# Optimization experiments

Measured on AMD Instinct MI355X. Metric: run time of the kernel, lower is better.

The kernel has to match this reference:

```python
import jax, jax.numpy as jnp
import numpy as np

NEG = -1e30  # finite stand-in for -inf so logaddexp grads stay clean
ADVERSARY_WEIGHT = 0.5


def _bfctc(logits, targets, act_lens, tgt_lens):
    """Blank-free CTC negative log-likelihood, size_average=True (mean over batch).

    logits: (T, B, C) unnormalized activations (log_softmax applied internally,
            as in warp-ctc style bindings).
    targets: (B, U) int label ids (padding beyond tgt_lens is ignored).
    Alignment lattice: at each frame stay on the same label or advance one
    label (no blank state):
        alpha[t, u] = logaddexp(alpha[t-1, u], alpha[t-1, u-1]) + logp[t, y_u]
    Loss per utterance = -alpha[act_len-1, tgt_len-1].
    """
    T, B, C = logits.shape
    U = targets.shape[1]
    logprobs = jax.nn.log_softmax(logits, axis=-1)  # (T,B,C)
    idx = jnp.broadcast_to(targets[None], (T, B, U))
    lp = jnp.take_along_axis(logprobs, idx, axis=2)  # (T,B,U) logp of each target label per frame

    alpha0 = lp[0] + jnp.where(jnp.arange(U) == 0, 0.0, NEG)[None, :]  # (B,U)

    def step(alpha, inp):
        lp_t, t = inp
        shifted = jnp.concatenate(
            [jnp.full((B, 1), NEG, alpha.dtype), alpha[:, :-1]], axis=1)
        new = jnp.logaddexp(alpha, shifted) + lp_t
        # freeze alpha once past this utterance's frame length
        alpha = jnp.where((t < act_lens)[:, None], new, alpha)
        return alpha, None

    alpha, _ = jax.lax.scan(step, alpha0, (lp[1:], jnp.arange(1, T)))
    loss_b = -jnp.take_along_axis(alpha, (tgt_lens - 1)[:, None], axis=1)[:, 0]
    return jnp.mean(loss_b)  # size_average=True


def reference(x, W, b, ctc_target_p1, ctc_target_p2, ctc_acts_lens,
              ctc_target_lens_p1, ctc_target_lens_p2):
    # output_layer projection then (B,T,C) -> (T,B,C), float32 cast
    logits = (x @ W + b)
    acts = jnp.transpose(logits, (1, 0, 2)).astype(jnp.float32)
    l1 = _bfctc(acts, ctc_target_p1, ctc_acts_lens, ctc_target_lens_p1)
    l2 = _bfctc(acts, ctc_target_p2, ctc_acts_lens, ctc_target_lens_p2)
    return (l1 - ADVERSARY_WEIGHT * l2, l1, l2)


def setup_inputs() -> dict:
    B, T, U, D, C = 16, 2000, 400, 512, 4096
    key = jax.random.key(0)
    k = jax.random.split(key, 8)
    x = jax.random.normal(k[0], (B, T, D), dtype=jnp.float32)
    W = jax.random.normal(k[1], (D, C), dtype=jnp.float32) * 0.02
    b = jnp.zeros((C,), dtype=jnp.float32)
    tgt1 = jax.random.randint(k[2], (B, U), 0, C)
    tgt2 = jax.random.randint(k[3], (B, U), 0, C)
    # frame lengths in [T//2, T) so every target (U<=400) has a valid alignment
    act_lens = jax.random.randint(k[4], (B,), T // 2, T)
    tlen1 = jax.random.randint(k[5], (B,), 1, U + 1)
    tlen2 = jax.random.randint(k[6], (B,), 1, U + 1)
    return {
        "x": x, "W": W, "b": b,
        "ctc_target_p1": tgt1, "ctc_target_p2": tgt2,
        "ctc_acts_lens": act_lens,
        "ctc_target_lens_p1": tlen1, "ctc_target_lens_p2": tlen2,
    }
```

## Files before the change

kernel.cpp:

```cpp
#include <hip/hip_runtime.h>
#include <hip/hip_bf16.h>
#include <stdint.h>

constexpr int B_ = 16;
constexpr int T_ = 2000;
constexpr int U_ = 400;
constexpr int D_ = 512;
constexpr int C_ = 4096;
constexpr int U2P_ = 1024;
constexpr float LN2F = 0.6931471805599453f;

typedef __attribute__((ext_vector_type(8))) short bf16x8;
typedef __attribute__((ext_vector_type(4))) float f32x4;
typedef __attribute__((ext_vector_type(8))) unsigned short us8;

__device__ __forceinline__ ushort f2bf(float f) {
  uint32_t u = __builtin_bit_cast(uint32_t, f);
  uint32_t r = (u + 0x7fffu + ((u >> 16) & 1u)) >> 16;
  return (ushort)r;
}

__device__ __forceinline__ float bf2f(ushort h) {
  return __builtin_bit_cast(float, (uint32_t)h << 16);
}

__device__ __forceinline__ void async_copy16(const void* gptr, void* ldsptr) {
  __builtin_amdgcn_global_load_lds(
      (const __attribute__((address_space(1))) uint32_t*)gptr,
      (__attribute__((address_space(3))) uint32_t*)ldsptr,
      16, 0, 0);
}

__global__ void cvt_bf16_k(const float* __restrict__ in, ushort* __restrict__ out, int n4) {
  int i = blockIdx.x * blockDim.x + threadIdx.x;
  int stride = gridDim.x * blockDim.x;
  for (; i < n4; i += stride) {
    float4 v = ((const float4*)in)[i];
    ushort4 o;
    o.x = f2bf(v.x); o.y = f2bf(v.y); o.z = f2bf(v.z); o.w = f2bf(v.w);
    ((ushort4*)out)[i] = o;
  }
}

__global__ void transposeW_k(const float* __restrict__ W, ushort* __restrict__ Wt) {
  __shared__ float tile[32][33];
  int c0 = blockIdx.x * 32, d0 = blockIdx.y * 32;
  int tx = threadIdx.x, ty = threadIdx.y;
  #pragma unroll
  for (int i = 0; i < 4; ++i) {
    int r = ty + i * 8;
    tile[r][tx] = W[(size_t)(d0 + r) * C_ + c0 + tx];
  }
  __syncthreads();
  #pragma unroll
  for (int i = 0; i < 4; ++i) {
    int r = ty + i * 8;
    Wt[(size_t)(c0 + r) * D_ + d0 + tx] = f2bf(tile[tx][r]);
  }
}

__global__ void gatherW_k(const ushort* __restrict__ Wt, const float* __restrict__ bias,
                          const int* __restrict__ t1, const int* __restrict__ t2,
                          ushort* __restrict__ Wgt, float* __restrict__ biasg) {
  int u2 = blockIdx.x;
  int b = blockIdx.y;
  int tid = threadIdx.x;
  int set = u2 >= 512;
  int us = u2 - (set ? 512 : 0);
  int c = (us < U_) ? (set ? t2 : t1)[b * U_ + us] : -1;
  ushort4 v; v.x = 0; v.y = 0; v.z = 0; v.w = 0;
  if (c >= 0) v = *(const ushort4*)(Wt + (size_t)c * D_ + tid * 4);
  *(ushort4*)(Wgt + ((size_t)b * U2P_ + u2) * D_ + tid * 4) = v;
  if (tid == 0) biasg[b * U2P_ + u2] = (c >= 0) ? bias[c] : 0.f;
}

template <bool IS_LP>
__global__ __launch_bounds__(512, 2) void gemm8_k(
    const ushort* __restrict__ A, const ushort* __restrict__ Bt,
    const float* __restrict__ biasp, float* __restrict__ lsesum,
    ushort* __restrict__ cbuf) {
  constexpr int K = D_;
  __shared__ __align__(16) ushort As[2][2][8192];
  __shared__ __align__(16) ushort Bs[2][2][8192];
  const int tid = threadIdx.x;
  const int wid = tid >> 6, lane = tid & 63;
  const int wr = wid >> 2, wc = wid & 3;
  const int h = lane >> 4, lr = lane & 15;
  const int bn = blockIdx.x, bm = blockIdx.y, bz = blockIdx.z;

  const ushort* Ab = A + ((size_t)(IS_LP ? bz * T_ : 0) + (size_t)bm * 256) * K;
  const ushort* Bb = Bt + ((size_t)(IS_LP ? bz * U2P_ : 0) + (size_t)bn * 256) * K;

  auto frag = [&](const ushort* chunk, int row) -> bf16x8 {
    int c16 = (h + (row >> 1)) & 3;
    return *(const bf16x8*)(chunk + row * 32 + c16 * 8);
  };
  auto stage = [&](ushort* chunk, const ushort* gsrc) {
    #pragma unroll
    for (int j = 0; j < 2; ++j) {
      int o = j * 512 + tid;
      int row = o >> 2;
      int g = ((o & 3) - (row >> 1)) & 3;
      async_copy16(gsrc + (size_t)row * K + g * 8,
                   chunk + (j * 512 + wid * 64) * 8);
    }
  };

  f32x4 acc[8][4];
  #pragma unroll
  for (int mi = 0; mi < 8; ++mi)
    #pragma unroll
    for (int ni = 0; ni < 4; ++ni) {
      f32x4 z = {0.f, 0.f, 0.f, 0.f};
      acc[mi][ni] = z;
    }

  stage(&As[0][0][0], Ab);
  stage(&Bs[0][0][0], Bb);
  stage(&As[0][1][0], Ab + 32);
  stage(&Bs[0][1][0], Bb + 32);

  #pragma unroll 2
  for (int kt = 0; kt < 8; ++kt) {
    const int c = kt & 1, nx = c ^ 1;
    const ushort* A0 = &As[c][0][0];
    const ushort* A1 = &As[c][1][0];
    const ushort* B0 = &Bs[c][0][0];
    const ushort* B1 = &Bs[c][1][0];
    const ushort* Asrc = Ab + (kt + 1) * 64;
    const ushort* Bsrc = Bb + (kt + 1) * 64;
    bf16x8 bf0[4], bf1[4], af[4];

    asm volatile("s_waitcnt vmcnt(4)" ::: "memory");
    __builtin_amdgcn_s_barrier();
    __builtin_amdgcn_sched_barrier(0);
    #pragma unroll
    for (int ni = 0; ni < 4; ++ni) bf0[ni] = frag(B0, wc * 64 + ni * 16 + lr);
    #pragma unroll
    for (int mi = 0; mi < 4; ++mi) af[mi] = frag(A0, wr * 128 + mi * 16 + lr);
    if (kt < 7) stage(&As[nx][0][0], Asrc);
    __builtin_amdgcn_s_setprio(1);
    #pragma unroll
    for (int mi = 0; mi < 4; ++mi)
      #pragma unroll
      for (int ni = 0; ni < 4; ++ni)
        acc[mi][ni] = __builtin_amdgcn_mfma_f32_16x16x32_bf16(af[mi], bf0[ni], acc[mi][ni], 0, 0, 0);
    __builtin_amdgcn_s_setprio(0);

    __builtin_amdgcn_s_barrier();
    __builtin_amdgcn_sched_barrier(0);
    #pragma unroll
    for (int mi = 0; mi < 4; ++mi) af[mi] = frag(A0, wr * 128 + (mi + 4) * 16 + lr);
    if (kt < 7) stage(&Bs[nx][0][0], Bsrc);
    __builtin_amdgcn_s_setprio(1);
    #pragma unroll
    for (int mi = 0; mi < 4; ++mi)
      #pragma unroll
      for (int ni = 0; ni < 4; ++ni)
        acc[mi + 4][ni] = __builtin_amdgcn_mfma_f32_16x16x32_bf16(af[mi], bf0[ni], acc[mi + 4][ni], 0, 0, 0);
    __builtin_amdgcn_s_setprio(0);

    if (kt < 7) { asm volatile("s_waitcnt vmcnt(4)" ::: "memory"); }
    else        { asm volatile("s_waitcnt vmcnt(0)" ::: "memory"); }
    __builtin_amdgcn_s_barrier();
    __builtin_amdgcn_sched_barrier(0);
    #pragma unroll
    for (int ni = 0; ni < 4; ++ni) bf1[ni] = frag(B1, wc * 64 + ni * 16 + lr);
    #pragma unroll
    for (int mi = 0; mi < 4; ++mi) af[mi] = frag(A1, wr * 128 + mi * 16 + lr);
    if (kt < 7) stage(&As[nx][1][0], Asrc + 32);
    __builtin_amdgcn_s_setprio(1);
    #pragma unroll
    for (int mi = 0; mi < 4; ++mi)
      #pragma unroll
      for (int ni = 0; ni < 4; ++ni)
        acc[mi][ni] = __builtin_amdgcn_mfma_f32_16x16x32_bf16(af[mi], bf1[ni], acc[mi][ni], 0, 0, 0);
    __builtin_amdgcn_s_setprio(0);

    __builtin_amdgcn_s_barrier();
    __builtin_amdgcn_sched_barrier(0);
    #pragma unroll
    for (int mi = 0; mi < 4; ++mi) af[mi] = frag(A1, wr * 128 + (mi + 4) * 16 + lr);
    if (kt < 7) stage(&Bs[nx][1][0], Bsrc + 32);
    __builtin_amdgcn_s_setprio(1);
    #pragma unroll
    for (int mi = 0; mi < 4; ++mi)
      #pragma unroll
      for (int ni = 0; ni < 4; ++ni)
        acc[mi + 4][ni] = __builtin_amdgcn_mfma_f32_16x16x32_bf16(af[mi], bf1[ni], acc[mi + 4][ni], 0, 0, 0);
    __builtin_amdgcn_s_setprio(0);
  }

  if constexpr (!IS_LP) {
    float bv[4];
    #pragma unroll
    for (int ni = 0; ni < 4; ++ni)
      bv[ni] = biasp[bn * 256 + wc * 64 + ni * 16 + lr];
    #pragma unroll
    for (int mi = 0; mi < 8; ++mi) {
      #pragma unroll
      for (int r = 0; r < 4; ++r) {
        float s = 0.f;
        #pragma unroll
        for (int ni = 0; ni < 4; ++ni) s += __expf(acc[mi][ni][r] + bv[ni]);
        s += __shfl_xor(s, 1);
        s += __shfl_xor(s, 2);
        s += __shfl_xor(s, 4);
        s += __shfl_xor(s, 8);
        if (lr == 0) {
          int grow = bm * 256 + wr * 128 + mi * 16 + h * 4 + r;
          atomicAdd(&lsesum[grow], s);
        }
      }
    }
  } else {
    float bv[4];
    #pragma unroll
    for (int ni = 0; ni < 4; ++ni)
      bv[ni] = biasp[bz * U2P_ + bn * 256 + wc * 64 + ni * 16 + lr];
    #pragma unroll
    for (int mi = 0; mi < 8; ++mi) {
      #pragma unroll
      for (int r = 0; r < 4; ++r) {
        int t = bm * 256 + wr * 128 + mi * 16 + h * 4 + r;
        if (t < T_) {
          #pragma unroll
          for (int ni = 0; ni < 4; ++ni) {
            int u2 = bn * 256 + wc * 64 + ni * 16 + lr;
            int set = u2 >> 9;
            int us = u2 & 511;
            float val = (us < U_) ? __expf(acc[mi][ni][r] + bv[ni]) : 0.f;
            cbuf[((size_t)(bz * 2 + set) * T_ + t) * 512 + us] = f2bf(val);
          }
        }
      }
    }
  }
}

__global__ void lse_reduce_k(const float* __restrict__ lsesum, const int* __restrict__ act_lens,
                             float* __restrict__ S) {
  int b = blockIdx.x;
  int al = act_lens[b];
  float s = 0.f;
  for (int t = threadIdx.x; t < al; t += blockDim.x)
    s += logf(lsesum[b * T_ + t]);
  #pragma unroll
  for (int off = 32; off >= 1; off >>= 1) s += __shfl_xor(s, off);
  __shared__ float wsum[4];
  int w = threadIdx.x >> 6, lane = threadIdx.x & 63;
  if (lane == 0) wsum[w] = s;
  __syncthreads();
  if (threadIdx.x == 0) S[b] = wsum[0] + wsum[1] + wsum[2] + wsum[3];
}

__global__ __launch_bounds__(64) void bfctc_scan_k(
    const ushort* __restrict__ cbuf, const int* __restrict__ act_lens,
    const int* __restrict__ tl1, const int* __restrict__ tl2,
    float* __restrict__ rawloss) {
  int bi = blockIdx.x;
  int b = bi >> 1, set = bi & 1;
  int lane = threadIdx.x;
  int al = act_lens[b];
  int tl = (set ? tl2 : tl1)[b];
  const char* base = (const char*)cbuf + (size_t)bi * T_ * 1024 + lane * 16;

  float alpha[8];
  int E = 0;
  float bscale;

  {
    us8 c0 = *(const us8*)(base);
    float iv0 = bf2f(c0[0]);
    #pragma unroll
    for (int r = 0; r < 8; ++r) alpha[r] = 0.f;
    if (lane == 0) alpha[0] = iv0;
    bscale = (lane >= 50) ? 0.f : 1.0f;
  }

  auto step1 = [&](us8 c8) {
    int pi = __builtin_amdgcn_update_dpp(
        0, __builtin_bit_cast(int, alpha[7]), 0x138 , 0xf, 0xf, true);
    float prev = __builtin_bit_cast(float, pi) * bscale;
    float c[8];
    #pragma unroll
    for (int r = 0; r < 8; ++r) c[r] = bf2f(c8[r]);
    #pragma unroll
    for (int r = 7; r >= 1; --r)
      alpha[r] = (alpha[r] + alpha[r - 1]) * c[r];
    alpha[0] = (alpha[0] + prev) * c[0];
  };

  auto rescale = [&]() {
    float m01 = fmaxf(alpha[0], alpha[1]);
    float m23 = fmaxf(alpha[2], alpha[3]);
    float m45 = fmaxf(alpha[4], alpha[5]);
    float m67 = fmaxf(alpha[6], alpha[7]);
    float m = fmaxf(fmaxf(m01, m23), fmaxf(m45, m67));
    int mb = __builtin_bit_cast(int, m);
    bool dead = (mb == 0);
    int ei = ((mb >> 23) & 255) - 127;
    float s = __builtin_bit_cast(float, (127 - ei) << 23);
    #pragma unroll
    for (int r = 0; r < 8; ++r) alpha[r] *= s;
    if (!dead) E += ei;
    int pe = __builtin_amdgcn_update_dpp(0, E, 0x138, 0xf, 0xf, true);
    if (dead) E = pe;
    int dE = pe - E;
    dE = dE < -126 ? -126 : (dE > 126 ? 126 : dE);
    bscale = __builtin_bit_cast(float, (127 + dE) << 23);
    if (lane >= 50) bscale = 0.f;
  };

  us8 B0[8], B1[8], B2[8], B3[8];
  auto load0 = [&](int blk) {
    const char* p = base + (size_t)(1 + 8 * blk) * 1024;
    #pragma unroll
    for (int i = 0; i < 8; ++i) B0[i] = *(const us8*)(p + i * 1024);
  };
  auto load1 = [&](int blk) {
    const char* p = base + (size_t)(1 + 8 * blk) * 1024;
    #pragma unroll
    for (int i = 0; i < 8; ++i) B1[i] = *(const us8*)(p + i * 1024);
  };
  auto load2 = [&](int blk) {
    const char* p = base + (size_t)(1 + 8 * blk) * 1024;
    #pragma unroll
    for (int i = 0; i < 8; ++i) B2[i] = *(const us8*)(p + i * 1024);
  };
  auto load3 = [&](int blk) {
    const char* p = base + (size_t)(1 + 8 * blk) * 1024;
    #pragma unroll
    for (int i = 0; i < 8; ++i) B3[i] = *(const us8*)(p + i * 1024);
  };
  auto comp0 = [&]() {
    #pragma unroll
    for (int i = 0; i < 8; ++i) step1(B0[i]);
  };
  auto comp1 = [&]() {
    #pragma unroll
    for (int i = 0; i < 8; ++i) step1(B1[i]);
  };
  auto comp2 = [&]() {
    #pragma unroll
    for (int i = 0; i < 8; ++i) step1(B2[i]);
  };
  auto comp3 = [&]() {
    #pragma unroll
    for (int i = 0; i < 8; ++i) step1(B3[i]);
  };

  int S = al - 1;
  int nb = S >> 3;
  load0(0); load1(1); load2(2); load3(3);
  int j = 0;
  while (j + 4 <= nb) {
    comp0(); rescale(); load0(j + 4);
    comp1(); rescale(); load1(j + 5);
    comp2(); rescale(); load2(j + 6);
    comp3(); rescale(); load3(j + 7);
    j += 4;
  }
  if (j < nb)     { comp0(); rescale(); }
  if (j + 1 < nb) { comp1(); rescale(); }
  if (j + 2 < nb) { comp2(); rescale(); }
  for (int t = 1 + 8 * nb; t <= S; ++t) {
    us8 c = *(const us8*)(base + (size_t)t * 1024);
    step1(c);
  }

  int ui = tl - 1, lt = ui >> 3, rt = ui & 7;
  float v = alpha[0];
  #pragma unroll
  for (int r = 1; r < 8; ++r) v = (rt == r) ? alpha[r] : v;
  float tot = (__builtin_amdgcn_logf(v) + (float)E) * LN2F;
  tot = __shfl(tot, lt);
  if (lane == 0) rawloss[bi] = tot;
}

__global__ void combine_k(const float* __restrict__ S, const float* __restrict__ raw,
                          float* __restrict__ out) {
  int lane = threadIdx.x;
  float d1 = 0.f, d2 = 0.f;
  if (lane < 16) {
    d1 = S[lane] - raw[lane * 2 + 0];
    d2 = S[lane] - raw[lane * 2 + 1];
  }
  #pragma unroll
  for (int off = 8; off >= 1; off >>= 1) {
    d1 += __shfl_xor(d1, off);
    d2 += __shfl_xor(d2, off);
  }
  if (lane == 0) {
    float l1 = d1 * (1.f / 16.f), l2 = d2 * (1.f / 16.f);
    out[0] = l1 - 0.5f * l2;
    out[1] = l1;
    out[2] = l2;
  }
}

extern "C" void kernel_launch(void* const* d_in, const int* in_sizes, int n_in,
                              void* d_out, int out_size, void* d_ws, size_t ws_size,
                              hipStream_t stream) {
  const float* x    = (const float*)d_in[0];
  const float* W    = (const float*)d_in[1];
  const float* bias = (const float*)d_in[2];
  const int* t1  = (const int*)d_in[3];
  const int* t2  = (const int*)d_in[4];
  const int* al  = (const int*)d_in[5];
  const int* tl1 = (const int*)d_in[6];
  const int* tl2 = (const int*)d_in[7];
  float* out = (float*)d_out;

  char* ws = (char*)d_ws;
  size_t off = 0;
  auto alloc = [&](size_t bytes) -> char* {
    char* p = ws + off;
    off += (bytes + 255) & ~(size_t)255;
    return p;
  };
  ushort* xb     = (ushort*)alloc((size_t)B_ * T_ * D_ * 2);
  ushort* Wt     = (ushort*)alloc((size_t)C_ * D_ * 2);
  ushort* Wgt    = (ushort*)alloc((size_t)B_ * U2P_ * D_ * 2);
  float*  biasg  = (float*)alloc((size_t)B_ * U2P_ * 4);
  float*  lsesum = (float*)alloc((size_t)B_ * T_ * 4);
  ushort* cbuf   = (ushort*)alloc((size_t)2 * B_ * T_ * 512 * 2);
  alloc(65536);
  float*  Sb     = (float*)alloc(B_ * 4);
  float*  rawl   = (float*)alloc(2 * B_ * 4);
  (void)ws_size; (void)in_sizes; (void)n_in; (void)out_size;

  (void)hipMemsetAsync(lsesum, 0, (size_t)B_ * T_ * 4, stream);

  cvt_bf16_k<<<2048, 256, 0, stream>>>(x, xb, B_ * T_ * D_ / 4);
  transposeW_k<<<dim3(C_ / 32, D_ / 32), dim3(32, 8), 0, stream>>>(W, Wt);
  gatherW_k<<<dim3(U2P_, B_), 128, 0, stream>>>(Wt, bias, t1, t2, Wgt, biasg);

  gemm8_k<false><<<dim3(C_ / 256, (B_ * T_) / 256, 1), 512, 0, stream>>>(
      xb, Wt, bias, lsesum, nullptr);
  gemm8_k<true><<<dim3(U2P_ / 256, 2048 / 256, B_), 512, 0, stream>>>(
      xb, Wgt, biasg, nullptr, cbuf);

  lse_reduce_k<<<B_, 256, 0, stream>>>(lsesum, al, Sb);
  bfctc_scan_k<<<2 * B_, 64, 0, stream>>>(cbuf, al, tl1, tl2, rawl);
  combine_k<<<1, 64, 0, stream>>>(Sb, rawl, out);
}
```

Measured before the change: 470.4 us.

## Make LSE GEMM blocks loop over eight N tiles with persistent row sums

```diff
diff --git a/kernel.cpp b/kernel.cpp
--- a/kernel.cpp
+++ b/kernel.cpp
@@ -74,11 +74,172 @@
   if (tid == 0) biasg[b * U2P_ + u2] = (c >= 0) ? bias[c] : 0.f;
 }
 
-template <bool IS_LP>
-__global__ __launch_bounds__(512, 2) void gemm8_k(
+__global__ __launch_bounds__(512, 2) void gemm_lse8_k(
     const ushort* __restrict__ A, const ushort* __restrict__ Bt,
-    const float* __restrict__ biasp, float* __restrict__ lsesum,
-    ushort* __restrict__ cbuf) {
+    const float* __restrict__ biasp, float* __restrict__ lsesum) {
+  constexpr int K = D_;
+  __shared__ __align__(16) ushort As[2][2][8192];
+  __shared__ __align__(16) ushort Bs[2][2][8192];
+  const int tid = threadIdx.x;
+  const int wid = tid >> 6, lane = tid & 63;
+  const int wr = wid >> 2, wc = wid & 3;
+  const int h = lane >> 4, lr = lane & 15;
+  const int nh = blockIdx.x;
+  const int bm = blockIdx.y;
+
+  const ushort* Ab = A + (size_t)bm * 256 * K;
+  const ushort* Bbase = Bt + (size_t)nh * 2048 * K;
+
+  auto frag = [&](const ushort* chunk, int row) -> bf16x8 {
+    int c16 = (h + (row >> 1)) & 3;
+    return *(const bf16x8*)(chunk + row * 32 + c16 * 8);
+  };
+  auto stage = [&](ushort* chunk, const ushort* gsrc) {
+    #pragma unroll
+    for (int j = 0; j < 2; ++j) {
+      int o = j * 512 + tid;
+      int row = o >> 2;
+      int g = ((o & 3) - (row >> 1)) & 3;
+      async_copy16(gsrc + (size_t)row * K + g * 8,
+                   chunk + (j * 512 + wid * 64) * 8);
+    }
+  };
+
+  f32x4 acc[8][4];
+  float rowsum[8][4];
+  #pragma unroll
+  for (int mi = 0; mi < 8; ++mi)
+    #pragma unroll
+    for (int ni = 0; ni < 4; ++ni) {
+      f32x4 z = {0.f, 0.f, 0.f, 0.f};
+      acc[mi][ni] = z;
+    }
+  #pragma unroll
+  for (int mi = 0; mi < 8; ++mi)
+    #pragma unroll
+    for (int r = 0; r < 4; ++r) rowsum[mi][r] = 0.f;
+
+  stage(&As[0][0][0], Ab);
+  stage(&Bs[0][0][0], Bbase);
+  stage(&As[0][1][0], Ab + 32);
+  stage(&Bs[0][1][0], Bbase + 32);
+
+  for (int i = 0; i < 64; ++i) {
+    const int c = i & 1, nx = c ^ 1;
+    const int kt1 = (i + 1) & 7, bn1 = (i + 1) >> 3;
+    const ushort* A0 = &As[c][0][0];
+    const ushort* A1 = &As[c][1][0];
+    const ushort* B0 = &Bs[c][0][0];
+    const ushort* B1 = &Bs[c][1][0];
+    const ushort* Asrc = Ab + kt1 * 64;
+    const ushort* Bsrc = Bbase + (size_t)bn1 * 256 * K + kt1 * 64;
+    bf16x8 bf0[4], bf1[4], af[4];
+
+    asm volatile("s_waitcnt vmcnt(4)" ::: "memory");
+    __builtin_amdgcn_s_barrier();
+    __builtin_amdgcn_sched_barrier(0);
+    #pragma unroll
+    for (int ni = 0; ni < 4; ++ni) bf0[ni] = frag(B0, wc * 64 + ni * 16 + lr);
+    #pragma unroll
+    for (int mi = 0; mi < 4; ++mi) af[mi] = frag(A0, wr * 128 + mi * 16 + lr);
+    if (i < 63) stage(&As[nx][0][0], Asrc);
+    __builtin_amdgcn_s_setprio(1);
+    #pragma unroll
+    for (int mi = 0; mi < 4; ++mi)
+      #pragma unroll
+      for (int ni = 0; ni < 4; ++ni)
+        acc[mi][ni] = __builtin_amdgcn_mfma_f32_16x16x32_bf16(af[mi], bf0[ni], acc[mi][ni], 0, 0, 0);
+    __builtin_amdgcn_s_setprio(0);
+
+    __builtin_amdgcn_s_barrier();
+    __builtin_amdgcn_sched_barrier(0);
+    #pragma unroll
+    for (int mi = 0; mi < 4; ++mi) af[mi] = frag(A0, wr * 128 + (mi + 4) * 16 + lr);
+    if (i < 63) stage(&Bs[nx][0][0], Bsrc);
+    __builtin_amdgcn_s_setprio(1);
+    #pragma unroll
+    for (int mi = 0; mi < 4; ++mi)
+      #pragma unroll
+      for (int ni = 0; ni < 4; ++ni)
+        acc[mi + 4][ni] = __builtin_amdgcn_mfma_f32_16x16x32_bf16(af[mi], bf0[ni], acc[mi + 4][ni], 0, 0, 0);
+    __builtin_amdgcn_s_setprio(0);
+
+    if (i < 63) { asm volatile("s_waitcnt vmcnt(4)" ::: "memory"); }
+    else        { asm volatile("s_waitcnt vmcnt(0)" ::: "memory"); }
+    __builtin_amdgcn_s_barrier();
+    __builtin_amdgcn_sched_barrier(0);
+    #pragma unroll
+    for (int ni = 0; ni < 4; ++ni) bf1[ni] = frag(B1, wc * 64 + ni * 16 + lr);
+    #pragma unroll
+    for (int mi = 0; mi < 4; ++mi) af[mi] = frag(A1, wr * 128 + mi * 16 + lr);
+    if (i < 63) stage(&As[nx][1][0], Asrc + 32);
+    __builtin_amdgcn_s_setprio(1);
+    #pragma unroll
+    for (int mi = 0; mi < 4; ++mi)
+      #pragma unroll
+      for (int ni = 0; ni < 4; ++ni)
+        acc[mi][ni] = __builtin_amdgcn_mfma_f32_16x16x32_bf16(af[mi], bf1[ni], acc[mi][ni], 0, 0, 0);
+    __builtin_amdgcn_s_setprio(0);
+
+    __builtin_amdgcn_s_barrier();
+    __builtin_amdgcn_sched_barrier(0);
+    #pragma unroll
+    for (int mi = 0; mi < 4; ++mi) af[mi] = frag(A1, wr * 128 + (mi + 4) * 16 + lr);
+    if (i < 63) stage(&Bs[nx][1][0], Bsrc + 32);
+    __builtin_amdgcn_s_setprio(1);
+    #pragma unroll
+    for (int mi = 0; mi < 4; ++mi)
+      #pragma unroll
+      for (int ni = 0; ni < 4; ++ni)
+        acc[mi + 4][ni] = __builtin_amdgcn_mfma_f32_16x16x32_bf16(af[mi], bf1[ni], acc[mi + 4][ni], 0, 0, 0);
+    __builtin_amdgcn_s_setprio(0);
+
+    if ((i & 7) == 7) {
+      int bn = i >> 3;
+      float bv[4];
+      #pragma unroll
+      for (int ni = 0; ni < 4; ++ni)
+        bv[ni] = biasp[nh * 2048 + bn * 256 + wc * 64 + ni * 16 + lr];
+      #pragma unroll
+      for (int mi = 0; mi < 8; ++mi) {
+        #pragma unroll
+        for (int r = 0; r < 4; ++r) {
+          float s = 0.f;
+          #pragma unroll
+          for (int ni = 0; ni < 4; ++ni) s += __expf(acc[mi][ni][r] + bv[ni]);
+          rowsum[mi][r] += s;
+        }
+      }
+      #pragma unroll
+      for (int mi = 0; mi < 8; ++mi)
+        #pragma unroll
+        for (int ni = 0; ni < 4; ++ni) {
+          f32x4 z = {0.f, 0.f, 0.f, 0.f};
+          acc[mi][ni] = z;
+        }
+    }
+  }
+
+  #pragma unroll
+  for (int mi = 0; mi < 8; ++mi) {
+    #pragma unroll
+    for (int r = 0; r < 4; ++r) {
+      float s = rowsum[mi][r];
+      s += __shfl_xor(s, 1);
+      s += __shfl_xor(s, 2);
+      s += __shfl_xor(s, 4);
+      s += __shfl_xor(s, 8);
+      if (lr == 0) {
+        int grow = bm * 256 + wr * 128 + mi * 16 + h * 4 + r;
+        atomicAdd(&lsesum[grow], s);
+      }
+    }
+  }
+}
+
+__global__ __launch_bounds__(512, 2) void gemm_lp8_k(
+    const ushort* __restrict__ A, const ushort* __restrict__ Bt,
+    const float* __restrict__ biasp, ushort* __restrict__ cbuf) {
   constexpr int K = D_;
   __shared__ __align__(16) ushort As[2][2][8192];
   __shared__ __align__(16) ushort Bs[2][2][8192];
@@ -88,8 +249,8 @@
   const int h = lane >> 4, lr = lane & 15;
   const int bn = blockIdx.x, bm = blockIdx.y, bz = blockIdx.z;
 
-  const ushort* Ab = A + ((size_t)(IS_LP ? bz * T_ : 0) + (size_t)bm * 256) * K;
-  const ushort* Bb = Bt + ((size_t)(IS_LP ? bz * U2P_ : 0) + (size_t)bn * 256) * K;
+  const ushort* Ab = A + ((size_t)bz * T_ + (size_t)bm * 256) * K;
+  const ushort* Bb = Bt + ((size_t)bz * U2P_ + (size_t)bn * 256) * K;
 
   auto frag = [&](const ushort* chunk, int row) -> bf16x8 {
     int c16 = (h + (row >> 1)) & 3;
@@ -191,47 +352,23 @@
     __builtin_amdgcn_s_setprio(0);
   }
 
-  if constexpr (!IS_LP) {
-    float bv[4];
-    #pragma unroll
-    for (int ni = 0; ni < 4; ++ni)
-      bv[ni] = biasp[bn * 256 + wc * 64 + ni * 16 + lr];
-    #pragma unroll
-    for (int mi = 0; mi < 8; ++mi) {
-      #pragma unroll
-      for (int r = 0; r < 4; ++r) {
-        float s = 0.f;
+  float bv[4];
+  #pragma unroll
+  for (int ni = 0; ni < 4; ++ni)
+    bv[ni] = biasp[bz * U2P_ + bn * 256 + wc * 64 + ni * 16 + lr];
+  #pragma unroll
+  for (int mi = 0; mi < 8; ++mi) {
+    #pragma unroll
+    for (int r = 0; r < 4; ++r) {
+      int t = bm * 256 + wr * 128 + mi * 16 + h * 4 + r;
+      if (t < T_) {
         #pragma unroll
-        for (int ni = 0; ni < 4; ++ni) s += __expf(acc[mi][ni][r] + bv[ni]);
-        s += __shfl_xor(s, 1);
-        s += __shfl_xor(s, 2);
-        s += __shfl_xor(s, 4);
-        s += __shfl_xor(s, 8);
-        if (lr == 0) {
-          int grow = bm * 256 + wr * 128 + mi * 16 + h * 4 + r;
-          atomicAdd(&lsesum[grow], s);
-        }
-      }
-    }
-  } else {
-    float bv[4];
-    #pragma unroll
-    for (int ni = 0; ni < 4; ++ni)
-      bv[ni] = biasp[bz * U2P_ + bn * 256 + wc * 64 + ni * 16 + lr];
-    #pragma unroll
-    for (int mi = 0; mi < 8; ++mi) {
-      #pragma unroll
-      for (int r = 0; r < 4; ++r) {
-        int t = bm * 256 + wr * 128 + mi * 16 + h * 4 + r;
-        if (t < T_) {
-          #pragma unroll
-          for (int ni = 0; ni < 4; ++ni) {
-            int u2 = bn * 256 + wc * 64 + ni * 16 + lr;
-            int set = u2 >> 9;
-            int us = u2 & 511;
-            float val = (us < U_) ? __expf(acc[mi][ni][r] + bv[ni]) : 0.f;
-            cbuf[((size_t)(bz * 2 + set) * T_ + t) * 512 + us] = f2bf(val);
-          }
+        for (int ni = 0; ni < 4; ++ni) {
+          int u2 = bn * 256 + wc * 64 + ni * 16 + lr;
+          int set = u2 >> 9;
+          int us = u2 & 511;
+          float val = (us < U_) ? __expf(acc[mi][ni][r] + bv[ni]) : 0.f;
+          cbuf[((size_t)(bz * 2 + set) * T_ + t) * 512 + us] = f2bf(val);
         }
       }
     }
@@ -436,10 +573,10 @@
   transposeW_k<<<dim3(C_ / 32, D_ / 32), dim3(32, 8), 0, stream>>>(W, Wt);
   gatherW_k<<<dim3(U2P_, B_), 128, 0, stream>>>(Wt, bias, t1, t2, Wgt, biasg);
 
-  gemm8_k<false><<<dim3(C_ / 256, (B_ * T_) / 256, 1), 512, 0, stream>>>(
-      xb, Wt, bias, lsesum, nullptr);
-  gemm8_k<true><<<dim3(U2P_ / 256, 2048 / 256, B_), 512, 0, stream>>>(
-      xb, Wgt, biasg, nullptr, cbuf);
+  gemm_lse8_k<<<dim3(2, (B_ * T_) / 256, 1), 512, 0, stream>>>(
+      xb, Wt, bias, lsesum);
+  gemm_lp8_k<<<dim3(U2P_ / 256, 2048 / 256, B_), 512, 0, stream>>>(
+      xb, Wgt, biasg, cbuf);
 
   lse_reduce_k<<<B_, 256, 0, stream>>>(lsesum, al, Sb);
   bfctc_scan_k<<<2 * B_, 64, 0, stream>>>(cbuf, al, tl1, tl2, rawl);
```

Result: faster. 456.7 us (-2.9%).
